# Kernel optimization log

Hardware: AMD Instinct MI355X
Metric: run time of the kernel (lower is better)

Reference implementation:

```python
import jax, jax.numpy as jnp
import numpy as np

B, S, H, OUT, L = 32, 4096, 128, 128, 3


def _log_g(x):
    return jnp.where(x >= 0, jnp.log(jax.nn.relu(x) + 0.5), -jax.nn.softplus(-x))


def _cell(x, Wz, bz, Wh, bh):
    # x: [B, S, Din] -> h: [B, S, H]
    k = x @ Wz.T + bz                              # [B,S,H]
    log_z = -jax.nn.softplus(-k)
    log_coeffs = -jax.nn.softplus(k)
    # h_0 = zeros -> log_g(0) = log(0.5)
    log_h0 = jnp.full((x.shape[0], 1, k.shape[-1]), np.log(0.5), dtype=k.dtype)
    log_tilde_h = _log_g(x @ Wh.T + bh)
    log_values = jnp.concatenate([log_h0, log_z + log_tilde_h], axis=1)  # [B,S+1,H]
    # FAITHFUL to source: cumsum over the FEATURE axis (dim=-1), pad along seq
    a_star = jnp.pad(jnp.cumsum(log_coeffs, axis=-1), ((0, 0), (1, 0), (0, 0)))
    log_h = a_star + jax.lax.cumlogsumexp(log_values - a_star, axis=1)
    # torch forward applies sigmoid to the cell output, then drops the h_0 row
    return jax.nn.sigmoid(jnp.exp(log_h))[:, 1:, :]


def setup_inputs() -> dict:
    key = jax.random.key(0)
    ks = jax.random.split(key, 2 * L + 2)
    inp = {"x": jax.random.normal(ks[0], (B, S), dtype=jnp.float32)}
    for l in range(L):
        din = 1 if l == 0 else H
        inp[f"Wz{l}"] = jax.random.normal(ks[1 + 2 * l], (H, din), dtype=jnp.float32) * 0.02
        inp[f"bz{l}"] = jnp.zeros((H,), dtype=jnp.float32)
        inp[f"Wh{l}"] = jax.random.normal(ks[2 + 2 * l], (H, din), dtype=jnp.float32) * 0.02
        inp[f"bh{l}"] = jnp.zeros((H,), dtype=jnp.float32)
    inp["Wout"] = jax.random.normal(ks[-1], (OUT, H * S), dtype=jnp.float32) * (1.0 / np.sqrt(H * S))
    inp["bout"] = jnp.zeros((OUT,), dtype=jnp.float32)
    return inp


def reference(x, Wz0, bz0, Wh0, bh0, Wz1, bz1, Wh1, bh1, Wz2, bz2, Wh2, bh2, Wout, bout):
    h = x[:, :, None]  # [B,S,1]
    for (Wz, bz, Wh, bh) in ((Wz0, bz0, Wh0, bh0), (Wz1, bz1, Wh1, bh1), (Wz2, bz2, Wh2, bh2)):
        h = _cell(h, Wz, bz, Wh, bh)
    flat = h.reshape(h.shape[0], -1)  # [B, S*H]
    return flat @ Wout.T + bout       # [B, OUT]
```

## Files before the change

kernel.cpp:

```cpp
#include <hip/hip_runtime.h>
#include <hip/hip_bf16.h>
#include <math.h>

#define B_   32
#define S_   4096
#define H_   128
#define OUT_ 128
#define P_   (B_*S_)
#define NC_  64
#define CH_  (S_/NC_)
#define NKS_ 512
#define KTOT_ (H_*S_)
#define NEGINF_ (-__builtin_inff())
#define HTP_ 136
#define LOGHALF_ (-0.6931471805599453f)

typedef __bf16 bf16x8 __attribute__((ext_vector_type(8)));
typedef float  f32x4  __attribute__((ext_vector_type(4)));
typedef unsigned short ushort8_t __attribute__((ext_vector_type(8)));

__device__ __forceinline__ float sp_(float x) {
  return __logf(1.f + __expf(x));
}
__device__ __forceinline__ float logg_(float x) {
  float t = (x >= 0.f) ? (x + 0.5f) : __builtin_amdgcn_rcpf(1.f + __expf(-x));
  return __logf(t);
}
__device__ __forceinline__ float lae_(float a, float b) {
  float m = fmaxf(a, b);
  float d = -fabsf(a - b);
  return m + __logf(1.f + __expf(d));
}
__device__ __forceinline__ float sigm_(float e) {
  return __builtin_amdgcn_rcpf(1.f + __expf(-e));
}
__device__ __forceinline__ unsigned short f2bf_(float f) {
  unsigned int u = __float_as_uint(f);
  u += 0x7fffu + ((u >> 16) & 1u);
  return (unsigned short)(u >> 16);
}

#define DPPADD_(v, ctrl, rmask) \
  ((v) + __int_as_float(__builtin_amdgcn_update_dpp( \
      0, __float_as_int(v), (ctrl), (rmask), 0xf, true)))
__device__ __forceinline__ float wscan_(float v) {
  v = DPPADD_(v, 0x111, 0xf);
  v = DPPADD_(v, 0x112, 0xf);
  v = DPPADD_(v, 0x114, 0xf);
  v = DPPADD_(v, 0x118, 0xf);
  v = DPPADD_(v, 0x142, 0xa);
  v = DPPADD_(v, 0x143, 0xc);
  return v;
}

__global__ __launch_bounds__(256) void prep0c_kernel(
    const float* __restrict__ x,
    const float* __restrict__ Wz, const float* __restrict__ bz,
    const float* __restrict__ Wh, const float* __restrict__ bh,
    float* __restrict__ u, float* __restrict__ A, float* __restrict__ tot,
    const float* __restrict__ Wz1, const float* __restrict__ Wh1,
    const float* __restrict__ Wz2, const float* __restrict__ Wh2,
    unsigned short* __restrict__ Wc1, unsigned short* __restrict__ Wc2)
{
  __shared__ float tpart[4][128];
  if (blockIdx.x >= 2048) {
    int idx = (blockIdx.x - 2048) * 256 + threadIdx.x;
    Wc1[idx] = f2bf_(idx < 16384 ? Wz1[idx] : Wh1[idx - 16384]);
    Wc2[idx] = f2bf_(idx < 16384 ? Wz2[idx] : Wh2[idx - 16384]);
    return;
  }
  int lane = threadIdx.x & 63, w = threadIdx.x >> 6;
  float wz0 = Wz[lane], wz1 = Wz[lane + 64];
  float bz0 = bz[lane], bz1 = bz[lane + 64];
  float wh0 = Wh[lane], wh1 = Wh[lane + 64];
  float bh0 = bh[lane], bh1 = bh[lane + 64];
  int blk = blockIdx.x;
  size_t base = (size_t)blk * (CH_ * H_);
  int pos0 = blk * CH_;
  float t0 = NEGINF_, t1 = NEGINF_;
  for (int j = 0; j < 16; ++j) {
    int i = j * 4 + w;
    float xv = x[pos0 + i];
    float k0 = fmaf(xv, wz0, bz0), k1 = fmaf(xv, wz1, bz1);
    float g0 = fmaf(xv, wh0, bh0), g1 = fmaf(xv, wh1, bh1);
    float lc0 = -sp_(k0), lc1 = -sp_(k1);
    float lv0 = k0 + lc0 + logg_(g0);
    float lv1 = k1 + lc1 + logg_(g1);
    float s0 = wscan_(lc0);
    float c0 = __shfl(s0, 63, 64);
    float s1 = wscan_(lc1) + c0;
    float u0 = lv0 - s0, u1 = lv1 - s1;
    size_t o = base + (size_t)i * H_;
    u[o + lane]      = u0;  u[o + 64 + lane] = u1;
    A[o + lane]      = s0;  A[o + 64 + lane] = s1;
    t0 = lae_(t0, u0); t1 = lae_(t1, u1);
  }
  tpart[w][lane] = t0; tpart[w][64 + lane] = t1;
  __syncthreads();
  if (w == 0) {
    int ch = lane;
    tot[(size_t)blk * H_ + ch] =
        lae_(lae_(tpart[0][ch], tpart[1][ch]), lae_(tpart[2][ch], tpart[3][ch]));
    ch = lane + 64;
    tot[(size_t)blk * H_ + ch] =
        lae_(lae_(tpart[0][ch], tpart[1][ch]), lae_(tpart[2][ch], tpart[3][ch]));
  }
}

__global__ __launch_bounds__(256) void kb_kernel(
    const float* __restrict__ totIn,
    const unsigned short* __restrict__ Wc,
    const float* __restrict__ bz, const float* __restrict__ bh,
    float* __restrict__ u, float* __restrict__ A,
    float* __restrict__ totOut)
{
  __shared__ unsigned short hT[64][HTP_];
  __shared__ union {
    float kg[16][260];
    float scr[32][128];
  } ks;
  __shared__ float thand[128];
  __shared__ float tpart[4][128];
  int tid = threadIdx.x;
  int lane = tid & 63, w = tid >> 6;
  int l15 = lane & 15, quad = lane >> 4;
  int half = tid >> 7, ch = tid & 127;
  int blk = blockIdx.x;
  int cidx = blk & (NC_ - 1);
  size_t base = (size_t)blk * (CH_ * H_);

  {
    const float* tp = totIn + (size_t)(blk - cidx) * H_ + ch;
    float p0 = NEGINF_, p1 = NEGINF_;
    int i = half;
    for (; i + 2 < cidx; i += 4) {
      float a0 = tp[(size_t)i * H_];
      float a1 = tp[(size_t)(i + 2) * H_];
      p0 = lae_(p0, a0); p1 = lae_(p1, a1);
    }
    for (; i < cidx; i += 2) p0 = lae_(p0, tp[(size_t)i * H_]);
    tpart[half * 2][ch] = p0; tpart[half * 2 + 1][ch] = p1;
  }
  __syncthreads();

  if (half == 0) {
    float r = LOGHALF_;
    r = lae_(r, tpart[0][ch]); r = lae_(r, tpart[1][ch]);
    r = lae_(r, tpart[2][ch]); r = lae_(r, tpart[3][ch]);
    const float* up = u + base + ch;
    const float* Ap = A + base + ch;
    for (int i0 = 0; i0 < 32; i0 += 16) {
      float uv[16], av[16];
      #pragma unroll
      for (int i = 0; i < 16; ++i) { uv[i] = up[(i0 + i) * H_]; av[i] = Ap[(i0 + i) * H_]; }
      #pragma unroll
      for (int i = 0; i < 16; ++i) {
        r = lae_(r, uv[i]);
        hT[i0 + i][ch] = f2bf_(sigm_(__expf(av[i] + r)));
      }
    }
    thand[ch] = r;
  } else {
    float r = NEGINF_;
    const float* up = u + base + ch;
    for (int i0 = 0; i0 < 32; i0 += 16) {
      float uv[16];
      #pragma unroll
      for (int i = 0; i < 16; ++i) uv[i] = up[(32 + i0 + i) * H_];
      #pragma unroll
      for (int i = 0; i < 16; ++i) { r = lae_(r, uv[i]); ks.scr[i0 + i][ch] = r; }
    }
  }
  __syncthreads();
  if (half == 1) {
    float r31 = thand[ch];
    const float* Ap = A + base + ch;
    for (int i0 = 0; i0 < 32; i0 += 16) {
      float av[16];
      #pragma unroll
      for (int i = 0; i < 16; ++i) av[i] = Ap[(32 + i0 + i) * H_];
      #pragma unroll
      for (int i = 0; i < 16; ++i) {
        float ri = lae_(r31, ks.scr[i0 + i][ch]);
        hT[32 + i0 + i][ch] = f2bf_(sigm_(__expf(av[i] + ri)));
      }
    }
  }
  __syncthreads();

  float bz0v = bz[lane], bz1v = bz[lane + 64];
  float bh0v = bh[lane], bh1v = bh[lane + 64];
  float t0 = NEGINF_, t1 = NEGINF_;

  for (int t = 0; t < 4; ++t) {
    f32x4 z = {0.f, 0.f, 0.f, 0.f};
    f32x4 acc[4] = {z, z, z, z};
    #pragma unroll
    for (int kk = 0; kk < 4; ++kk) {
      bf16x8 a = *reinterpret_cast<const bf16x8*>(&hT[t * 16 + l15][kk * 32 + quad * 8]);
      #pragma unroll
      for (int nt = 0; nt < 4; ++nt) {
        int n = w * 64 + nt * 16 + l15;
        bf16x8 bf = *reinterpret_cast<const bf16x8*>(Wc + n * 128 + kk * 32 + quad * 8);
        acc[nt] = __builtin_amdgcn_mfma_f32_16x16x32_bf16(a, bf, acc[nt], 0, 0, 0);
      }
    }
    __syncthreads();
    #pragma unroll
    for (int nt = 0; nt < 4; ++nt) {
      int col = w * 64 + nt * 16 + l15;
      #pragma unroll
      for (int r2 = 0; r2 < 4; ++r2)
        ks.kg[quad * 4 + r2][col] = acc[nt][r2];
    }
    __syncthreads();
    #pragma unroll
    for (int i = 0; i < 4; ++i) {
      int row = w + i * 4;
      int sIdx = t * 16 + row;
      float k0 = ks.kg[row][lane]        + bz0v;
      float k1 = ks.kg[row][64 + lane]   + bz1v;
      float g0 = ks.kg[row][128 + lane]  + bh0v;
      float g1 = ks.kg[row][192 + lane]  + bh1v;
      float lc0 = -sp_(k0), lc1 = -sp_(k1);
      float lv0 = k0 + lc0 + logg_(g0);
      float lv1 = k1 + lc1 + logg_(g1);
      float s0 = wscan_(lc0);
      float c0 = __shfl(s0, 63, 64);
      float s1 = wscan_(lc1) + c0;
      float u0 = lv0 - s0, u1 = lv1 - s1;
      size_t o = base + (size_t)sIdx * H_;
      u[o + lane]      = u0;  u[o + 64 + lane] = u1;
      A[o + lane]      = s0;  A[o + 64 + lane] = s1;
      t0 = lae_(t0, u0); t1 = lae_(t1, u1);
    }
  }

  tpart[w][lane] = t0; tpart[w][64 + lane] = t1;
  __syncthreads();
  if (w == 0) {
    int c = lane;
    totOut[(size_t)blk * H_ + c] =
        lae_(lae_(tpart[0][c], tpart[1][c]), lae_(tpart[2][c], tpart[3][c]));
    c = lane + 64;
    totOut[(size_t)blk * H_ + c] =
        lae_(lae_(tpart[0][c], tpart[1][c]), lae_(tpart[2][c], tpart[3][c]));
  }
}

__global__ __launch_bounds__(256) void scan3v2_kernel(
    const float* __restrict__ u, const float* __restrict__ A,
    const float* __restrict__ totIn, unsigned short* __restrict__ hbf)
{
  __shared__ float scr[32][128];
  __shared__ float thand[128];
  __shared__ float tpart[4][128];
  int tid = threadIdx.x;
  int half = tid >> 7, ch = tid & 127;
  int blk = blockIdx.x;
  int cidx = blk & (NC_ - 1);
  size_t base = (size_t)blk * (CH_ * H_);
  const float* up = u + base + ch;
  const float* Ap = A + base + ch;
  unsigned short* hp = hbf + base + ch;

  {
    const float* tp = totIn + (size_t)(blk - cidx) * H_ + ch;
    float p0 = NEGINF_, p1 = NEGINF_;
    int i = half;
    for (; i + 2 < cidx; i += 4) {
      float a0 = tp[(size_t)i * H_];
      float a1 = tp[(size_t)(i + 2) * H_];
      p0 = lae_(p0, a0); p1 = lae_(p1, a1);
    }
    for (; i < cidx; i += 2) p0 = lae_(p0, tp[(size_t)i * H_]);
    tpart[half * 2][ch] = p0; tpart[half * 2 + 1][ch] = p1;
  }
  __syncthreads();

  if (half == 0) {
    float r = LOGHALF_;
    r = lae_(r, tpart[0][ch]); r = lae_(r, tpart[1][ch]);
    r = lae_(r, tpart[2][ch]); r = lae_(r, tpart[3][ch]);
    for (int i0 = 0; i0 < 32; i0 += 16) {
      float uv[16], av[16];
      #pragma unroll
      for (int i = 0; i < 16; ++i) { uv[i] = up[(i0 + i) * H_]; av[i] = Ap[(i0 + i) * H_]; }
      #pragma unroll
      for (int i = 0; i < 16; ++i) {
        r = lae_(r, uv[i]);
        hp[(size_t)(i0 + i) * H_] = f2bf_(sigm_(__expf(av[i] + r)));
      }
    }
    thand[ch] = r;
  } else {
    float r = NEGINF_;
    for (int i0 = 0; i0 < 32; i0 += 16) {
      float uv[16];
      #pragma unroll
      for (int i = 0; i < 16; ++i) uv[i] = up[(32 + i0 + i) * H_];
      #pragma unroll
      for (int i = 0; i < 16; ++i) { r = lae_(r, uv[i]); scr[i0 + i][ch] = r; }
    }
  }
  __syncthreads();
  if (half == 1) {
    float r31 = thand[ch];
    for (int i0 = 0; i0 < 32; i0 += 16) {
      float av[16];
      #pragma unroll
      for (int i = 0; i < 16; ++i) av[i] = Ap[(32 + i0 + i) * H_];
      #pragma unroll
      for (int i = 0; i < 16; ++i) {
        float ri = lae_(r31, scr[i0 + i][ch]);
        hp[(size_t)(32 + i0 + i) * H_] = f2bf_(sigm_(__expf(av[i] + ri)));
      }
    }
  }
}

__global__ __launch_bounds__(256) void outmm_kernel(
    const unsigned short* __restrict__ hbf,
    const float* __restrict__ Wout,
    float* __restrict__ part)
{
  const int KSL = KTOT_ / NKS_;
  int tid = threadIdx.x, w = tid >> 6, lane = tid & 63;
  int l15 = lane & 15, quad = lane >> 4;
  int k0base = blockIdx.x * KSL;
  f32x4 acc[2][2] = {{{0,0,0,0},{0,0,0,0}},{{0,0,0,0},{0,0,0,0}}};
  for (int ks = 0; ks < KSL; ks += 32) {
    int k0 = k0base + ks;
    bf16x8 a0 = *reinterpret_cast<const bf16x8*>(
        hbf + (size_t)l15 * KTOT_ + k0 + quad * 8);
    bf16x8 a1 = *reinterpret_cast<const bf16x8*>(
        hbf + (size_t)(16 + l15) * KTOT_ + k0 + quad * 8);
    #pragma unroll
    for (int nt = 0; nt < 2; ++nt) {
      int n = w * 32 + nt * 16 + l15;
      const float* wp = Wout + (size_t)n * KTOT_ + k0 + quad * 8;
      float4 wa = *reinterpret_cast<const float4*>(wp);
      float4 wb = *reinterpret_cast<const float4*>(wp + 4);
      ushort8_t tt;
      tt[0] = f2bf_(wa.x); tt[1] = f2bf_(wa.y); tt[2] = f2bf_(wa.z); tt[3] = f2bf_(wa.w);
      tt[4] = f2bf_(wb.x); tt[5] = f2bf_(wb.y); tt[6] = f2bf_(wb.z); tt[7] = f2bf_(wb.w);
      bf16x8 bf = __builtin_bit_cast(bf16x8, tt);
      acc[0][nt] = __builtin_amdgcn_mfma_f32_16x16x32_bf16(a0, bf, acc[0][nt], 0, 0, 0);
      acc[1][nt] = __builtin_amdgcn_mfma_f32_16x16x32_bf16(a1, bf, acc[1][nt], 0, 0, 0);
    }
  }
  float* pp = part + (size_t)blockIdx.x * (B_ * OUT_);
  #pragma unroll
  for (int mt = 0; mt < 2; ++mt)
    #pragma unroll
    for (int nt = 0; nt < 2; ++nt)
      #pragma unroll
      for (int r = 0; r < 4; ++r) {
        int b = mt * 16 + quad * 4 + r;
        int o = w * 32 + nt * 16 + l15;
        pp[b * OUT_ + o] = acc[mt][nt][r];
      }
}

__global__ __launch_bounds__(256) void outred_kernel(
    const float* __restrict__ part, const float* __restrict__ bout,
    float* __restrict__ out)
{
  int w = threadIdx.x >> 6, lane = threadIdx.x & 63;
  int idx = blockIdx.x * 4 + w;
  float s = 0.f;
  for (int wg = lane; wg < NKS_; wg += 64) s += part[(size_t)wg * (B_ * OUT_) + idx];
  #pragma unroll
  for (int d = 32; d; d >>= 1) s += __shfl_down(s, (unsigned)d, 64);
  if (lane == 0) out[idx] = s + bout[idx & (OUT_ - 1)];
}

extern "C" void kernel_launch(void* const* d_in, const int* in_sizes, int n_in,
                              void* d_out, int out_size, void* d_ws, size_t ws_size,
                              hipStream_t stream)
{
  const float* x    = (const float*)d_in[0];
  const float* Wz[3] = {(const float*)d_in[1], (const float*)d_in[5], (const float*)d_in[9]};
  const float* bz[3] = {(const float*)d_in[2], (const float*)d_in[6], (const float*)d_in[10]};
  const float* Wh[3] = {(const float*)d_in[3], (const float*)d_in[7], (const float*)d_in[11]};
  const float* bh[3] = {(const float*)d_in[4], (const float*)d_in[8], (const float*)d_in[12]};
  const float* Wout = (const float*)d_in[13];
  const float* bout = (const float*)d_in[14];
  float* out = (float*)d_out;

  char* ws = (char*)d_ws;
  float*          u     = (float*)(ws + 0);
  float*          A     = (float*)(ws + 67108864);
  unsigned short* hbf   = (unsigned short*)(ws + 134217728);
  unsigned short* Wc1   = (unsigned short*)(ws + 167772160);
  unsigned short* Wc2   = (unsigned short*)(ws + 167837696);
  float*          totA  = (float*)(ws + 167903232);
  float*          totB  = (float*)(ws + 168951808);
  float*          part  = (float*)(ws + 170000384);

  prep0c_kernel<<<B_ * NC_ + 128, 256, 0, stream>>>(
      x, Wz[0], bz[0], Wh[0], bh[0], u, A, totA,
      Wz[1], Wh[1], Wz[2], Wh[2], Wc1, Wc2);

  kb_kernel<<<B_ * NC_, 256, 0, stream>>>(totA, Wc1, bz[1], bh[1], u, A, totB);
  kb_kernel<<<B_ * NC_, 256, 0, stream>>>(totB, Wc2, bz[2], bh[2], u, A, totA);

  scan3v2_kernel<<<B_ * NC_, 256, 0, stream>>>(u, A, totA, hbf);

  outmm_kernel<<<NKS_, 256, 0, stream>>>(hbf, Wout, part);
  outred_kernel<<<(B_ * OUT_) / 4, 256, 0, stream>>>(part, bout, out);
}
```

Before: 658.6 us.

## Prefetch loads across kernels: hoist x loads, full-chunk scan loads, double-buffer outmm, coalesce outred

prep0c now loads all 16 x values before its compute loop and unrolls that loop. The chunked scan phases in kb and scan3 issue all 32 u/A loads at once instead of two batches of 16. outmm double-buffers its hbf and Wout loads so the next k-step's global reads are in flight while MFMAs run. outred is reorganized so each lane reads a contiguous output index (coalesced) and reduces through shared memory. The intent is more memory-level parallelism and less load latency exposure, at the cost of higher register pressure that may reduce occupancy.

Result: no change. 662.4 us (+0.6%).

```diff
diff --git a/kernel.cpp b/kernel.cpp
--- a/kernel.cpp
+++ b/kernel.cpp
@@ -77,12 +77,15 @@
   int blk = blockIdx.x;
   size_t base = (size_t)blk * (CH_ * H_);
   int pos0 = blk * CH_;
+  float xv[16];
+  #pragma unroll
+  for (int j = 0; j < 16; ++j) xv[j] = x[pos0 + j * 4 + w];
   float t0 = NEGINF_, t1 = NEGINF_;
+  #pragma unroll
   for (int j = 0; j < 16; ++j) {
     int i = j * 4 + w;
-    float xv = x[pos0 + i];
-    float k0 = fmaf(xv, wz0, bz0), k1 = fmaf(xv, wz1, bz1);
-    float g0 = fmaf(xv, wh0, bh0), g1 = fmaf(xv, wh1, bh1);
+    float k0 = fmaf(xv[j], wz0, bz0), k1 = fmaf(xv[j], wz1, bz1);
+    float g0 = fmaf(xv[j], wh0, bh0), g1 = fmaf(xv[j], wh1, bh1);
     float lc0 = -sp_(k0), lc1 = -sp_(k1);
     float lv0 = k0 + lc0 + logg_(g0);
     float lv1 = k1 + lc1 + logg_(g1);
@@ -149,41 +152,37 @@
     r = lae_(r, tpart[2][ch]); r = lae_(r, tpart[3][ch]);
     const float* up = u + base + ch;
     const float* Ap = A + base + ch;
-    for (int i0 = 0; i0 < 32; i0 += 16) {
-      float uv[16], av[16];
-      #pragma unroll
-      for (int i = 0; i < 16; ++i) { uv[i] = up[(i0 + i) * H_]; av[i] = Ap[(i0 + i) * H_]; }
-      #pragma unroll
-      for (int i = 0; i < 16; ++i) {
-        r = lae_(r, uv[i]);
-        hT[i0 + i][ch] = f2bf_(sigm_(__expf(av[i] + r)));
-      }
+    float uv[32], av[32];
+    #pragma unroll
+    for (int i = 0; i < 32; ++i) uv[i] = up[i * H_];
+    #pragma unroll
+    for (int i = 0; i < 32; ++i) av[i] = Ap[i * H_];
+    #pragma unroll
+    for (int i = 0; i < 32; ++i) {
+      r = lae_(r, uv[i]);
+      hT[i][ch] = f2bf_(sigm_(__expf(av[i] + r)));
     }
     thand[ch] = r;
   } else {
     float r = NEGINF_;
     const float* up = u + base + ch;
-    for (int i0 = 0; i0 < 32; i0 += 16) {
-      float uv[16];
-      #pragma unroll
-      for (int i = 0; i < 16; ++i) uv[i] = up[(32 + i0 + i) * H_];
-      #pragma unroll
-      for (int i = 0; i < 16; ++i) { r = lae_(r, uv[i]); ks.scr[i0 + i][ch] = r; }
-    }
+    float uv[32];
+    #pragma unroll
+    for (int i = 0; i < 32; ++i) uv[i] = up[(32 + i) * H_];
+    #pragma unroll
+    for (int i = 0; i < 32; ++i) { r = lae_(r, uv[i]); ks.scr[i][ch] = r; }
   }
   __syncthreads();
   if (half == 1) {
     float r31 = thand[ch];
     const float* Ap = A + base + ch;
-    for (int i0 = 0; i0 < 32; i0 += 16) {
-      float av[16];
-      #pragma unroll
-      for (int i = 0; i < 16; ++i) av[i] = Ap[(32 + i0 + i) * H_];
-      #pragma unroll
-      for (int i = 0; i < 16; ++i) {
-        float ri = lae_(r31, ks.scr[i0 + i][ch]);
-        hT[32 + i0 + i][ch] = f2bf_(sigm_(__expf(av[i] + ri)));
-      }
+    float av[32];
+    #pragma unroll
+    for (int i = 0; i < 32; ++i) av[i] = Ap[(32 + i) * H_];
+    #pragma unroll
+    for (int i = 0; i < 32; ++i) {
+      float ri = lae_(r31, ks.scr[i][ch]);
+      hT[32 + i][ch] = f2bf_(sigm_(__expf(av[i] + ri)));
     }
   }
   __syncthreads();
@@ -282,40 +281,65 @@
     float r = LOGHALF_;
     r = lae_(r, tpart[0][ch]); r = lae_(r, tpart[1][ch]);
     r = lae_(r, tpart[2][ch]); r = lae_(r, tpart[3][ch]);
-    for (int i0 = 0; i0 < 32; i0 += 16) {
-      float uv[16], av[16];
-      #pragma unroll
-      for (int i = 0; i < 16; ++i) { uv[i] = up[(i0 + i) * H_]; av[i] = Ap[(i0 + i) * H_]; }
-      #pragma unroll
-      for (int i = 0; i < 16; ++i) {
-        r = lae_(r, uv[i]);
-        hp[(size_t)(i0 + i) * H_] = f2bf_(sigm_(__expf(av[i] + r)));
-      }
+    float uv[32], av[32];
+    #pragma unroll
+    for (int i = 0; i < 32; ++i) uv[i] = up[i * H_];
+    #pragma unroll
+    for (int i = 0; i < 32; ++i) av[i] = Ap[i * H_];
+    #pragma unroll
+    for (int i = 0; i < 32; ++i) {
+      r = lae_(r, uv[i]);
+      hp[(size_t)i * H_] = f2bf_(sigm_(__expf(av[i] + r)));
     }
     thand[ch] = r;
   } else {
     float r = NEGINF_;
-    for (int i0 = 0; i0 < 32; i0 += 16) {
-      float uv[16];
-      #pragma unroll
-      for (int i = 0; i < 16; ++i) uv[i] = up[(32 + i0 + i) * H_];
-      #pragma unroll
-      for (int i = 0; i < 16; ++i) { r = lae_(r, uv[i]); scr[i0 + i][ch] = r; }
-    }
+    float uv[32];
+    #pragma unroll
+    for (int i = 0; i < 32; ++i) uv[i] = up[(32 + i) * H_];
+    #pragma unroll
+    for (int i = 0; i < 32; ++i) { r = lae_(r, uv[i]); scr[i][ch] = r; }
   }
   __syncthreads();
   if (half == 1) {
     float r31 = thand[ch];
-    for (int i0 = 0; i0 < 32; i0 += 16) {
-      float av[16];
-      #pragma unroll
-      for (int i = 0; i < 16; ++i) av[i] = Ap[(32 + i0 + i) * H_];
-      #pragma unroll
-      for (int i = 0; i < 16; ++i) {
-        float ri = lae_(r31, scr[i0 + i][ch]);
-        hp[(size_t)(32 + i0 + i) * H_] = f2bf_(sigm_(__expf(av[i] + ri)));
-      }
-    }
+    float av[32];
+    #pragma unroll
+    for (int i = 0; i < 32; ++i) av[i] = Ap[(32 + i) * H_];
+    #pragma unroll
+    for (int i = 0; i < 32; ++i) {
+      float ri = lae_(r31, scr[i][ch]);
+      hp[(size_t)(32 + i) * H_] = f2bf_(sigm_(__expf(av[i] + ri)));
+    }
+  }
+}
+
+__device__ __forceinline__ void omload_(
+    const unsigned short* ap0, const unsigned short* ap1,
+    const float* wp0, const float* wp1, int k,
+    bf16x8& a0r, bf16x8& a1r, float4 (&wr)[2][2])
+{
+  a0r = *reinterpret_cast<const bf16x8*>(ap0 + k);
+  a1r = *reinterpret_cast<const bf16x8*>(ap1 + k);
+  wr[0][0] = *reinterpret_cast<const float4*>(wp0 + k);
+  wr[0][1] = *reinterpret_cast<const float4*>(wp0 + k + 4);
+  wr[1][0] = *reinterpret_cast<const float4*>(wp1 + k);
+  wr[1][1] = *reinterpret_cast<const float4*>(wp1 + k + 4);
+}
+__device__ __forceinline__ void omstep_(
+    const bf16x8& a0r, const bf16x8& a1r,
+    const float4 (&wr)[2][2], f32x4 (&acc)[2][2])
+{
+  #pragma unroll
+  for (int nt = 0; nt < 2; ++nt) {
+    ushort8_t tt;
+    tt[0] = f2bf_(wr[nt][0].x); tt[1] = f2bf_(wr[nt][0].y);
+    tt[2] = f2bf_(wr[nt][0].z); tt[3] = f2bf_(wr[nt][0].w);
+    tt[4] = f2bf_(wr[nt][1].x); tt[5] = f2bf_(wr[nt][1].y);
+    tt[6] = f2bf_(wr[nt][1].z); tt[7] = f2bf_(wr[nt][1].w);
+    bf16x8 bf = __builtin_bit_cast(bf16x8, tt);
+    acc[0][nt] = __builtin_amdgcn_mfma_f32_16x16x32_bf16(a0r, bf, acc[0][nt], 0, 0, 0);
+    acc[1][nt] = __builtin_amdgcn_mfma_f32_16x16x32_bf16(a1r, bf, acc[1][nt], 0, 0, 0);
   }
 }
 
@@ -328,26 +352,19 @@
   int tid = threadIdx.x, w = tid >> 6, lane = tid & 63;
   int l15 = lane & 15, quad = lane >> 4;
   int k0base = blockIdx.x * KSL;
+  const unsigned short* ap0 = hbf + (size_t)l15 * KTOT_ + k0base + quad * 8;
+  const unsigned short* ap1 = hbf + (size_t)(16 + l15) * KTOT_ + k0base + quad * 8;
+  const float* wp0 = Wout + (size_t)(w * 32 + l15) * KTOT_ + k0base + quad * 8;
+  const float* wp1 = Wout + (size_t)(w * 32 + 16 + l15) * KTOT_ + k0base + quad * 8;
   f32x4 acc[2][2] = {{{0,0,0,0},{0,0,0,0}},{{0,0,0,0},{0,0,0,0}}};
-  for (int ks = 0; ks < KSL; ks += 32) {
-    int k0 = k0base + ks;
-    bf16x8 a0 = *reinterpret_cast<const bf16x8*>(
-        hbf + (size_t)l15 * KTOT_ + k0 + quad * 8);
-    bf16x8 a1 = *reinterpret_cast<const bf16x8*>(
-        hbf + (size_t)(16 + l15) * KTOT_ + k0 + quad * 8);
-    #pragma unroll
-    for (int nt = 0; nt < 2; ++nt) {
-      int n = w * 32 + nt * 16 + l15;
-      const float* wp = Wout + (size_t)n * KTOT_ + k0 + quad * 8;
-      float4 wa = *reinterpret_cast<const float4*>(wp);
-      float4 wb = *reinterpret_cast<const float4*>(wp + 4);
-      ushort8_t tt;
-      tt[0] = f2bf_(wa.x); tt[1] = f2bf_(wa.y); tt[2] = f2bf_(wa.z); tt[3] = f2bf_(wa.w);
-      tt[4] = f2bf_(wb.x); tt[5] = f2bf_(wb.y); tt[6] = f2bf_(wb.z); tt[7] = f2bf_(wb.w);
-      bf16x8 bf = __builtin_bit_cast(bf16x8, tt);
-      acc[0][nt] = __builtin_amdgcn_mfma_f32_16x16x32_bf16(a0, bf, acc[0][nt], 0, 0, 0);
-      acc[1][nt] = __builtin_amdgcn_mfma_f32_16x16x32_bf16(a1, bf, acc[1][nt], 0, 0, 0);
-    }
+  bf16x8 aA0, aA1, aB0, aB1;
+  float4 wvA[2][2], wvB[2][2];
+  omload_(ap0, ap1, wp0, wp1, 0, aA0, aA1, wvA);
+  for (int ks = 0; ks < KSL; ks += 64) {
+    omload_(ap0, ap1, wp0, wp1, ks + 32, aB0, aB1, wvB);
+    omstep_(aA0, aA1, wvA, acc);
+    if (ks + 64 < KSL) omload_(ap0, ap1, wp0, wp1, ks + 64, aA0, aA1, wvA);
+    omstep_(aB0, aB1, wvB, acc);
   }
   float* pp = part + (size_t)blockIdx.x * (B_ * OUT_);
   #pragma unroll
@@ -366,13 +383,19 @@
     const float* __restrict__ part, const float* __restrict__ bout,
     float* __restrict__ out)
 {
+  __shared__ float red[4][64];
   int w = threadIdx.x >> 6, lane = threadIdx.x & 63;
-  int idx = blockIdx.x * 4 + w;
+  int idx0 = blockIdx.x * 64;
   float s = 0.f;
-  for (int wg = lane; wg < NKS_; wg += 64) s += part[(size_t)wg * (B_ * OUT_) + idx];
-  #pragma unroll
-  for (int d = 32; d; d >>= 1) s += __shfl_down(s, (unsigned)d, 64);
-  if (lane == 0) out[idx] = s + bout[idx & (OUT_ - 1)];
+  for (int wg = w; wg < NKS_; wg += 4)
+    s += part[(size_t)wg * (B_ * OUT_) + idx0 + lane];
+  red[w][lane] = s;
+  __syncthreads();
+  if (w == 0) {
+    float r = (red[0][lane] + red[1][lane]) + (red[2][lane] + red[3][lane]);
+    int idx = idx0 + lane;
+    out[idx] = r + bout[idx & (OUT_ - 1)];
+  }
 }
 
 extern "C" void kernel_launch(void* const* d_in, const int* in_sizes, int n_in,
@@ -408,5 +431,5 @@
   scan3v2_kernel<<<B_ * NC_, 256, 0, stream>>>(u, A, totA, hbf);
 
   outmm_kernel<<<NKS_, 256, 0, stream>>>(hbf, Wout, part);
-  outred_kernel<<<(B_ * OUT_) / 4, 256, 0, stream>>>(part, bout, out);
-}
+  outred_kernel<<<(B_ * OUT_) / 64, 256, 0, stream>>>(part, bout, out);
+}
```
